# Optimization experiments

Measured on AMD Instinct MI355X. Metric: run time of the kernel, lower is better.

Reference implementation:

```python
import jax, jax.numpy as jnp
import numpy as np

D_MODEL = 1024
N_HEADS = 16
TREE_DEPTH = 5
B, T = 2, 1024


def setup_inputs() -> dict:
    key = jax.random.key(0)
    k1, k2, k3, k4 = jax.random.split(key, 4)
    sc = 1.0 / np.sqrt(D_MODEL)
    return {
        "x": jax.random.normal(k1, (B, T, D_MODEL), dtype=jnp.float32),
        "Wp": jax.random.normal(k2, (D_MODEL, N_HEADS * TREE_DEPTH), dtype=jnp.float32) * sc,
        "bp": jnp.zeros((N_HEADS * TREE_DEPTH,), dtype=jnp.float32),
        "Wv": jax.random.normal(k3, (D_MODEL, D_MODEL), dtype=jnp.float32) * sc,
        "Wo": jax.random.normal(k4, (D_MODEL, D_MODEL), dtype=jnp.float32) * sc,
    }


def reference(x, Wp, bp, Wv, Wo):
    Bc, Tc, d = x.shape
    H, Dt = N_HEADS, TREE_DEPTH
    dh = d // H
    # tree paths: (B, H, T, Dt)
    paths = jax.nn.sigmoid(x @ Wp + bp).reshape(Bc, Tc, H, Dt).transpose(0, 2, 1, 3)
    pq = paths[:, :, :, None, :]  # (B,H,T,1,Dt)
    pk = paths[:, :, None, :, :]  # (B,H,1,T,Dt)
    agree = pq * pk + (1.0 - pq) * (1.0 - pk)  # (B,H,T,T,Dt)
    sim = jnp.cumprod(agree, axis=-1).sum(axis=-1) / Dt  # (B,H,T,T)
    # causal mask (strict upper triangle -> -inf)
    causal_mask = jnp.triu(jnp.ones((Tc, Tc), dtype=bool), k=1)
    sim = jnp.where(causal_mask[None, None], -jnp.inf, sim)
    attn = jax.nn.softmax(sim, axis=-1)
    V = (x @ Wv).reshape(Bc, Tc, H, dh).transpose(0, 2, 1, 3)  # (B,H,T,dh)
    ctx = jnp.einsum("bhqk,bhkd->bhqd", attn, V)
    ctx = ctx.transpose(0, 2, 1, 3).reshape(Bc, Tc, d)
    return ctx @ Wo
```

## Files before the change

kernel.cpp:

```cpp
#include <hip/hip_runtime.h>
#include <hip/hip_bf16.h>

#define B_SZ 2
#define T_SEQ 1024
#define D_MODEL 1024
#define N_HEADS 16
#define TREE_DEPTH 5
#define DH 64

typedef __attribute__((ext_vector_type(8))) short short8;
typedef __attribute__((ext_vector_type(4))) float f32x4;

__device__ __forceinline__ ushort f2bf(float f) {
    uint32_t u = __float_as_uint(f);
    u += 0x7FFFu + ((u >> 16) & 1u);
    return (ushort)(u >> 16);
}

__device__ __forceinline__ void gll16(const void* g, void* l) {
    __builtin_amdgcn_global_load_lds(
        (const __attribute__((address_space(1))) void*)g,
        (__attribute__((address_space(3))) void*)l, 16, 0, 0);
}

__global__ __launch_bounds__(256) void prologue(
    const float* __restrict__ x, const float* __restrict__ Wv,
    const float* __restrict__ Wo, const float* __restrict__ Wp,
    ushort* __restrict__ xb, ushort* __restrict__ Wvt,
    ushort* __restrict__ Wot, ushort* __restrict__ Wpt)
{
    __shared__ __align__(16) char sm[20480];
    const int bid = blockIdx.x, tid = threadIdx.x;
    if (bid < 1024) {
        const int i = (bid * 256 + tid) * 8;
        const float4 a = *(const float4*)(x + i);
        const float4 b = *(const float4*)(x + i + 4);
        ushort o[8] = {f2bf(a.x), f2bf(a.y), f2bf(a.z), f2bf(a.w),
                       f2bf(b.x), f2bf(b.y), f2bf(b.z), f2bf(b.w)};
        *(uint4*)(xb + i) = *(const uint4*)o;
    } else if (bid < 3072) {
        const int t = bid - 1024;
        const float* W = (t < 1024) ? Wv : Wo;
        ushort* Wt = (t < 1024) ? Wvt : Wot;
        const int ti = t & 1023;
        const int n0 = (ti & 31) * 32, k0 = (ti >> 5) * 32;
        float (*tile)[33] = (float(*)[33])sm;
        const int tx = tid & 31, ty = tid >> 5;
        #pragma unroll
        for (int i = 0; i < 4; ++i)
            tile[ty + i * 8][tx] = W[(size_t)(k0 + ty + i * 8) * 1024 + n0 + tx];
        __syncthreads();
        #pragma unroll
        for (int i = 0; i < 4; ++i)
            Wt[(size_t)(n0 + ty + i * 8) * 1024 + k0 + tx] = f2bf(tile[tx][ty + i * 8]);
    } else {
        float* tile = (float*)sm;
        const int k0 = (bid - 3072) * 64;
        #pragma unroll
        for (int j = 0; j < 20; ++j) {
            const int i = tid + j * 256;
            tile[i] = Wp[(size_t)k0 * 80 + i];
        }
        __syncthreads();
        #pragma unroll
        for (int j = 0; j < 20; ++j) {
            const int o = tid + j * 256;
            const int n = o >> 6, k = o & 63;
            Wpt[(size_t)n * 1024 + k0 + k] = f2bf(tile[k * 80 + n]);
        }
    }
}

template <bool OUT_BF16>
__device__ __forceinline__ void gemm_body(
    const ushort* __restrict__ A, const ushort* __restrict__ Bt,
    void* __restrict__ Cv, int N, int K, int bx, int by,
    ushort* As, ushort* Bs)
{
    const int tid = threadIdx.x;
    const int lane = tid & 63;
    const int w = tid >> 6;
    const int wm = w & 1, wn = w >> 1;
    const int rowBase = by * 64;
    const int colBase = bx * 64;

    const int srow = lane & 15;
    const int sk = (lane >> 4) * 8;

    const ushort* gA = A + (size_t)(rowBase + w * 16 + srow) * K + sk;
    const ushort* gB = Bt + (size_t)(colBase + w * 16 + srow) * K + sk;

    f32x4 acc[2][2];
    #pragma unroll
    for (int i = 0; i < 2; ++i) {
        acc[i][0] = (f32x4)0.0f;
        acc[i][1] = (f32x4)0.0f;
    }

    gll16(gA,      As + (w * 2 + 0) * 512);
    gll16(gA + 32, As + (w * 2 + 1) * 512);
    gll16(gB,      Bs + (w * 2 + 0) * 512);
    gll16(gB + 32, Bs + (w * 2 + 1) * 512);

    const int niter = K / 64;
    for (int it = 0; it < niter; ++it) {
        __syncthreads();
        const int cur = (it & 1) * 4096;
        if (it + 1 < niter) {
            const int nxt = ((it + 1) & 1) * 4096;
            const int ko = (it + 1) * 64;
            gll16(gA + ko,      As + nxt + (w * 2 + 0) * 512);
            gll16(gA + ko + 32, As + nxt + (w * 2 + 1) * 512);
            gll16(gB + ko,      Bs + nxt + (w * 2 + 0) * 512);
            gll16(gB + ko + 32, Bs + nxt + (w * 2 + 1) * 512);
        }
        #pragma unroll
        for (int ks = 0; ks < 2; ++ks) {
            short8 af[2], bf[2];
            #pragma unroll
            for (int i = 0; i < 2; ++i)
                af[i] = *(const short8*)(As + cur + ((wm * 2 + i) * 2 + ks) * 512 + lane * 8);
            #pragma unroll
            for (int j = 0; j < 2; ++j)
                bf[j] = *(const short8*)(Bs + cur + ((wn * 2 + j) * 2 + ks) * 512 + lane * 8);
            #pragma unroll
            for (int i = 0; i < 2; ++i)
                #pragma unroll
                for (int j = 0; j < 2; ++j)
                    acc[i][j] = __builtin_amdgcn_mfma_f32_16x16x32_bf16(
                        af[i], bf[j], acc[i][j], 0, 0, 0);
        }
    }

    const int quad = lane >> 4, m16 = lane & 15;
    #pragma unroll
    for (int i = 0; i < 2; ++i)
        #pragma unroll
        for (int j = 0; j < 2; ++j) {
            const int col = colBase + wn * 32 + j * 16 + m16;
            #pragma unroll
            for (int r = 0; r < 4; ++r) {
                const int row = rowBase + wm * 32 + i * 16 + quad * 4 + r;
                if (OUT_BF16)
                    ((ushort*)Cv)[(size_t)row * N + col] = f2bf(acc[i][j][r]);
                else
                    ((float*)Cv)[(size_t)row * N + col] = acc[i][j][r];
            }
        }
}

__device__ __forceinline__ void phi_body(
    const ushort* __restrict__ xb, const ushort* __restrict__ Wpt,
    const float* __restrict__ bp, ushort* __restrict__ Phi,
    int blk, float* red, float* p_s)
{
    const int tid = threadIdx.x;
    const int lane = tid & 63, w = tid >> 6;
    const int quad = lane >> 4, m16 = lane & 15;
    const int row0 = blk * 16;

    f32x4 acc[5];
    #pragma unroll
    for (int nb = 0; nb < 5; ++nb) acc[nb] = (f32x4)0.0f;

    const ushort* ap = xb + (size_t)(row0 + m16) * 1024 + w * 256 + quad * 8;
    const ushort* bpz = Wpt + (size_t)m16 * 1024 + w * 256 + quad * 8;
    #pragma unroll
    for (int it = 0; it < 8; ++it) {
        const short8 af = *(const short8*)(ap + it * 32);
        #pragma unroll
        for (int nb = 0; nb < 5; ++nb) {
            const short8 bf = *(const short8*)(bpz + (size_t)nb * 16 * 1024 + it * 32);
            acc[nb] = __builtin_amdgcn_mfma_f32_16x16x32_bf16(af, bf, acc[nb], 0, 0, 0);
        }
    }
    #pragma unroll
    for (int nb = 0; nb < 5; ++nb)
        #pragma unroll
        for (int r = 0; r < 4; ++r)
            red[(w * 16 + quad * 4 + r) * 80 + nb * 16 + m16] = acc[nb][r];
    __syncthreads();
    #pragma unroll
    for (int j = 0; j < 5; ++j) {
        const int i = tid + j * 256;
        const int rr = i / 80, cc = i - rr * 80;
        const float v = red[(0 * 16 + rr) * 80 + cc] + red[(1 * 16 + rr) * 80 + cc] +
                        red[(2 * 16 + rr) * 80 + cc] + red[(3 * 16 + rr) * 80 + cc] + bp[cc];
        p_s[rr * 80 + cc] = 1.0f / (1.0f + __expf(-v));
    }
    __syncthreads();
    #pragma unroll
    for (int j = 0; j < 8; ++j) {
        const int c = tid + j * 256;
        const int rr = c >> 7, rem = c & 127;
        const int h = rem >> 3, f8 = (rem & 7) * 8;
        const float* pr = &p_s[rr * 80 + h * 5];
        ushort o[8];
        #pragma unroll
        for (int e = 0; e < 8; ++e) {
            const int f = f8 + e;
            float val = 0.0f;
            if (f < 62) {
                int d, off;
                if (f < 2)       { d = 1; off = 0; }
                else if (f < 6)  { d = 2; off = 2; }
                else if (f < 14) { d = 3; off = 6; }
                else if (f < 30) { d = 4; off = 14; }
                else             { d = 5; off = 30; }
                const int e2 = f - off;
                float prod = 1.0f;
                for (int jj = 1; jj <= d; ++jj) {
                    const float p = pr[jj - 1];
                    prod *= ((e2 >> (d - jj)) & 1) ? (1.0f - p) : p;
                }
                val = prod;
            }
            o[e] = f2bf(val);
        }
        const int grow = row0 + rr;
        const int b = grow >> 10, t = grow & 1023;
        *(uint4*)(Phi + ((size_t)(b * 16 + h) * 1024 + t) * 64 + f8) =
            *(const uint4*)o;
    }
}

__global__ __launch_bounds__(256) void mid_kernel(
    const ushort* __restrict__ xb, const ushort* __restrict__ Wvt,
    const ushort* __restrict__ Wpt, const float* __restrict__ bp,
    ushort* __restrict__ Vt, ushort* __restrict__ Phi)
{
    __shared__ __align__(16) char sm[32768];
    if (blockIdx.x < 512) {
        ushort* As = (ushort*)sm;
        ushort* Bs = As + 8192;
        gemm_body<true>(Wvt, xb, Vt, 2048, 1024,
                        blockIdx.x & 31, blockIdx.x >> 5, As, Bs);
    } else {
        float* red = (float*)sm;
        float* p_s = (float*)(sm + 20480);
        phi_body(xb, Wpt, bp, Phi, blockIdx.x - 512, red, p_s);
    }
}

__global__ __launch_bounds__(256) void gemm_out(
    const ushort* __restrict__ ctxb, const ushort* __restrict__ Wot,
    float* __restrict__ out)
{
    __shared__ __align__(16) ushort sm[16384];
    gemm_body<false>(ctxb, Wot, out, 1024, 1024,
                     blockIdx.x, blockIdx.y, sm, sm + 8192);
}

__global__ __launch_bounds__(256) void attn_mfma(
    const ushort* __restrict__ Phi, const ushort* __restrict__ Vt,
    ushort* __restrict__ ctxb)
{
    const int qt = 15 - blockIdx.x;
    const int bh = blockIdx.y;
    const int b = bh >> 4, h = bh & 15;
    const int tid = threadIdx.x;
    const int lane = tid & 63;
    const int w = tid >> 6;
    const int quad = lane >> 4, m16 = lane & 15;

    __shared__ __align__(16) ushort K_s[2][4096];
    __shared__ __align__(16) ushort V_s[2][4096];
    __shared__ __align__(16) ushort W_s[4096];
    __shared__ float den_s[4][16];

    const int srow = lane & 15;
    const int sk = (lane >> 4) * 8;
    const ushort* gK = Phi + (size_t)bh * 1024 * 64 + (w * 16 + srow) * 64 + sk;
    const ushort* gV = Vt + (size_t)(h * 64 + w * 16 + srow) * 2048 + b * 1024 + sk;

    const int qglob = qt * 64 + w * 16 + m16;
    const ushort* qbase = Phi + ((size_t)bh * 1024 + qglob) * 64 + quad * 8;
    const short8 qf0 = *(const short8*)qbase;
    const short8 qf1 = *(const short8*)(qbase + 32);

    f32x4 cacc[4];
    #pragma unroll
    for (int nb = 0; nb < 4; ++nb) cacc[nb] = (f32x4)0.0f;
    float den = 0.0f;

    gll16(gK,      K_s[0] + (w * 2 + 0) * 512);
    gll16(gK + 32, K_s[0] + (w * 2 + 1) * 512);
    gll16(gV,      V_s[0] + (w * 2 + 0) * 512);
    gll16(gV + 32, V_s[0] + (w * 2 + 1) * 512);

    for (int kt = 0; kt <= qt; ++kt) {
        const int cur = kt & 1;
        __syncthreads();
        if (kt < qt) {
            const int nxt = cur ^ 1;
            const ushort* nK = gK + (kt + 1) * 4096;
            const ushort* nV = gV + (kt + 1) * 64;
            gll16(nK,      K_s[nxt] + (w * 2 + 0) * 512);
            gll16(nK + 32, K_s[nxt] + (w * 2 + 1) * 512);
            gll16(nV,      V_s[nxt] + (w * 2 + 0) * 512);
            gll16(nV + 32, V_s[nxt] + (w * 2 + 1) * 512);
        }
        #pragma unroll
        for (int nb = 0; nb < 4; ++nb) {
            const short8 kf0 = *(const short8*)(K_s[cur] + (nb * 2 + 0) * 512 + lane * 8);
            const short8 kf1 = *(const short8*)(K_s[cur] + (nb * 2 + 1) * 512 + lane * 8);
            f32x4 s = (f32x4)0.0f;
            s = __builtin_amdgcn_mfma_f32_16x16x32_bf16(kf0, qf0, s, 0, 0, 0);
            s = __builtin_amdgcn_mfma_f32_16x16x32_bf16(kf1, qf1, s, 0, 0, 0);
            const int k0g = kt * 64 + nb * 16 + quad * 4;
            ushort o[4];
            #pragma unroll
            for (int r = 0; r < 4; ++r) {
                float wgt = 0.0f;
                if (k0g + r <= qglob) wgt = __expf(s[r] * 0.2f);
                den += wgt;
                o[r] = f2bf(wgt);
            }
            const int addr = (w * 2 + (nb >> 1)) * 512 +
                             ((nb & 1) * 2 + (quad >> 1)) * 128 +
                             m16 * 8 + (quad & 1) * 4;
            *(uint2*)(W_s + addr) = *(const uint2*)o;
        }
        __syncthreads();
        const short8 wf0 = *(const short8*)(W_s + (w * 2 + 0) * 512 + lane * 8);
        const short8 wf1 = *(const short8*)(W_s + (w * 2 + 1) * 512 + lane * 8);
        #pragma unroll
        for (int nb = 0; nb < 4; ++nb) {
            const short8 vf0 = *(const short8*)(V_s[cur] + (nb * 2 + 0) * 512 + lane * 8);
            const short8 vf1 = *(const short8*)(V_s[cur] + (nb * 2 + 1) * 512 + lane * 8);
            cacc[nb] = __builtin_amdgcn_mfma_f32_16x16x32_bf16(wf0, vf0, cacc[nb], 0, 0, 0);
            cacc[nb] = __builtin_amdgcn_mfma_f32_16x16x32_bf16(wf1, vf1, cacc[nb], 0, 0, 0);
        }
    }

    den += __shfl_xor(den, 16);
    den += __shfl_xor(den, 32);
    den_s[w][m16] = den;
    __syncthreads();
    float inv[4];
    #pragma unroll
    for (int r = 0; r < 4; ++r) inv[r] = 1.0f / den_s[w][quad * 4 + r];

    #pragma unroll
    for (int nb = 0; nb < 4; ++nb) {
        const int dim = h * 64 + nb * 16 + m16;
        #pragma unroll
        for (int r = 0; r < 4; ++r) {
            const int token = qt * 64 + w * 16 + quad * 4 + r;
            ctxb[(size_t)(b * 1024 + token) * D_MODEL + dim] = f2bf(cacc[nb][r] * inv[r]);
        }
    }
}

extern "C" void kernel_launch(void* const* d_in, const int* in_sizes, int n_in,
                              void* d_out, int out_size, void* d_ws, size_t ws_size,
                              hipStream_t stream)
{
    const float* x  = (const float*)d_in[0];
    const float* Wp = (const float*)d_in[1];
    const float* bp = (const float*)d_in[2];
    const float* Wv = (const float*)d_in[3];
    const float* Wo = (const float*)d_in[4];
    float* out = (float*)d_out;

    char* ws = (char*)d_ws;
    ushort* xb   = (ushort*)(ws);
    ushort* Wvt  = (ushort*)(ws + (4u  << 20));
    ushort* Wot  = (ushort*)(ws + (6u  << 20));
    ushort* Phi  = (ushort*)(ws + (8u  << 20));
    ushort* Vt   = (ushort*)(ws + (12u << 20));
    ushort* ctxb = (ushort*)(ws + (16u << 20));
    ushort* Wpt  = (ushort*)(ws + (20u << 20));

    prologue<<<3088, 256, 0, stream>>>(x, Wv, Wo, Wp, xb, Wvt, Wot, Wpt);
    mid_kernel<<<640, 256, 0, stream>>>(xb, Wvt, Wpt, bp, Vt, Phi);
    attn_mfma<<<dim3(16, 32), 256, 0, stream>>>(Phi, Vt, ctxb);
    gemm_out<<<dim3(16, 32), 256, 0, stream>>>(ctxb, Wot, out);
}
```

Baseline: 151.5 us.

## Fuse all four stages into one cooperative persistent kernel with grid syncs

Replaces the four separate launches (convert/transpose prologue, V-projection plus phi, attention, output GEMM) with one cooperative kernel of 512 blocks that loops over the work and separates stages with grid.sync(). The goal is to remove per-launch overhead and tail gaps between kernels. It also changes the attention tile order so each block gets a mix of long and short causal tiles. The cost is grid-wide barriers, a fixed grid of 512 that must stay co-resident (launch bounds request 2 blocks per CU), and uneven work in the mid stage, where blocks 384 and above run both a GEMM tile and the phi computation.

```diff
diff --git a/kernel.cpp b/kernel.cpp
--- a/kernel.cpp
+++ b/kernel.cpp
@@ -1,5 +1,6 @@
 #include <hip/hip_runtime.h>
 #include <hip/hip_bf16.h>
+#include <hip/hip_cooperative_groups.h>
 
 #define B_SZ 2
 #define T_SEQ 1024
@@ -21,54 +22,6 @@
     __builtin_amdgcn_global_load_lds(
         (const __attribute__((address_space(1))) void*)g,
         (__attribute__((address_space(3))) void*)l, 16, 0, 0);
-}
-
-__global__ __launch_bounds__(256) void prologue(
-    const float* __restrict__ x, const float* __restrict__ Wv,
-    const float* __restrict__ Wo, const float* __restrict__ Wp,
-    ushort* __restrict__ xb, ushort* __restrict__ Wvt,
-    ushort* __restrict__ Wot, ushort* __restrict__ Wpt)
-{
-    __shared__ __align__(16) char sm[20480];
-    const int bid = blockIdx.x, tid = threadIdx.x;
-    if (bid < 1024) {
-        const int i = (bid * 256 + tid) * 8;
-        const float4 a = *(const float4*)(x + i);
-        const float4 b = *(const float4*)(x + i + 4);
-        ushort o[8] = {f2bf(a.x), f2bf(a.y), f2bf(a.z), f2bf(a.w),
-                       f2bf(b.x), f2bf(b.y), f2bf(b.z), f2bf(b.w)};
-        *(uint4*)(xb + i) = *(const uint4*)o;
-    } else if (bid < 3072) {
-        const int t = bid - 1024;
-        const float* W = (t < 1024) ? Wv : Wo;
-        ushort* Wt = (t < 1024) ? Wvt : Wot;
-        const int ti = t & 1023;
-        const int n0 = (ti & 31) * 32, k0 = (ti >> 5) * 32;
-        float (*tile)[33] = (float(*)[33])sm;
-        const int tx = tid & 31, ty = tid >> 5;
-        #pragma unroll
-        for (int i = 0; i < 4; ++i)
-            tile[ty + i * 8][tx] = W[(size_t)(k0 + ty + i * 8) * 1024 + n0 + tx];
-        __syncthreads();
-        #pragma unroll
-        for (int i = 0; i < 4; ++i)
-            Wt[(size_t)(n0 + ty + i * 8) * 1024 + k0 + tx] = f2bf(tile[tx][ty + i * 8]);
-    } else {
-        float* tile = (float*)sm;
-        const int k0 = (bid - 3072) * 64;
-        #pragma unroll
-        for (int j = 0; j < 20; ++j) {
-            const int i = tid + j * 256;
-            tile[i] = Wp[(size_t)k0 * 80 + i];
-        }
-        __syncthreads();
-        #pragma unroll
-        for (int j = 0; j < 20; ++j) {
-            const int o = tid + j * 256;
-            const int n = o >> 6, k = o & 63;
-            Wpt[(size_t)n * 1024 + k0 + k] = f2bf(tile[k * 80 + n]);
-        }
-    }
 }
 
 template <bool OUT_BF16>
@@ -224,50 +177,17 @@
     }
 }
 
-__global__ __launch_bounds__(256) void mid_kernel(
-    const ushort* __restrict__ xb, const ushort* __restrict__ Wvt,
-    const ushort* __restrict__ Wpt, const float* __restrict__ bp,
-    ushort* __restrict__ Vt, ushort* __restrict__ Phi)
-{
-    __shared__ __align__(16) char sm[32768];
-    if (blockIdx.x < 512) {
-        ushort* As = (ushort*)sm;
-        ushort* Bs = As + 8192;
-        gemm_body<true>(Wvt, xb, Vt, 2048, 1024,
-                        blockIdx.x & 31, blockIdx.x >> 5, As, Bs);
-    } else {
-        float* red = (float*)sm;
-        float* p_s = (float*)(sm + 20480);
-        phi_body(xb, Wpt, bp, Phi, blockIdx.x - 512, red, p_s);
-    }
-}
-
-__global__ __launch_bounds__(256) void gemm_out(
-    const ushort* __restrict__ ctxb, const ushort* __restrict__ Wot,
-    float* __restrict__ out)
-{
-    __shared__ __align__(16) ushort sm[16384];
-    gemm_body<false>(ctxb, Wot, out, 1024, 1024,
-                     blockIdx.x, blockIdx.y, sm, sm + 8192);
-}
-
-__global__ __launch_bounds__(256) void attn_mfma(
+__device__ __forceinline__ void attn_body(
     const ushort* __restrict__ Phi, const ushort* __restrict__ Vt,
-    ushort* __restrict__ ctxb)
-{
-    const int qt = 15 - blockIdx.x;
-    const int bh = blockIdx.y;
+    ushort* __restrict__ ctxb, int qt, int bh,
+    ushort* K_s0, ushort* V_s0, ushort* W_s, float* den_s)
+{
     const int b = bh >> 4, h = bh & 15;
     const int tid = threadIdx.x;
     const int lane = tid & 63;
     const int w = tid >> 6;
     const int quad = lane >> 4, m16 = lane & 15;
 
-    __shared__ __align__(16) ushort K_s[2][4096];
-    __shared__ __align__(16) ushort V_s[2][4096];
-    __shared__ __align__(16) ushort W_s[4096];
-    __shared__ float den_s[4][16];
-
     const int srow = lane & 15;
     const int sk = (lane >> 4) * 8;
     const ushort* gK = Phi + (size_t)bh * 1024 * 64 + (w * 16 + srow) * 64 + sk;
@@ -283,27 +203,27 @@
     for (int nb = 0; nb < 4; ++nb) cacc[nb] = (f32x4)0.0f;
     float den = 0.0f;
 
-    gll16(gK,      K_s[0] + (w * 2 + 0) * 512);
-    gll16(gK + 32, K_s[0] + (w * 2 + 1) * 512);
-    gll16(gV,      V_s[0] + (w * 2 + 0) * 512);
-    gll16(gV + 32, V_s[0] + (w * 2 + 1) * 512);
+    gll16(gK,      K_s0 + (w * 2 + 0) * 512);
+    gll16(gK + 32, K_s0 + (w * 2 + 1) * 512);
+    gll16(gV,      V_s0 + (w * 2 + 0) * 512);
+    gll16(gV + 32, V_s0 + (w * 2 + 1) * 512);
 
     for (int kt = 0; kt <= qt; ++kt) {
-        const int cur = kt & 1;
+        const int cur = (kt & 1) * 4096;
         __syncthreads();
         if (kt < qt) {
-            const int nxt = cur ^ 1;
+            const int nxt = ((kt + 1) & 1) * 4096;
             const ushort* nK = gK + (kt + 1) * 4096;
             const ushort* nV = gV + (kt + 1) * 64;
-            gll16(nK,      K_s[nxt] + (w * 2 + 0) * 512);
-            gll16(nK + 32, K_s[nxt] + (w * 2 + 1) * 512);
-            gll16(nV,      V_s[nxt] + (w * 2 + 0) * 512);
-            gll16(nV + 32, V_s[nxt] + (w * 2 + 1) * 512);
+            gll16(nK,      K_s0 + nxt + (w * 2 + 0) * 512);
+            gll16(nK + 32, K_s0 + nxt + (w * 2 + 1) * 512);
+            gll16(nV,      V_s0 + nxt + (w * 2 + 0) * 512);
+            gll16(nV + 32, V_s0 + nxt + (w * 2 + 1) * 512);
         }
         #pragma unroll
         for (int nb = 0; nb < 4; ++nb) {
-            const short8 kf0 = *(const short8*)(K_s[cur] + (nb * 2 + 0) * 512 + lane * 8);
-            const short8 kf1 = *(const short8*)(K_s[cur] + (nb * 2 + 1) * 512 + lane * 8);
+            const short8 kf0 = *(const short8*)(K_s0 + cur + (nb * 2 + 0) * 512 + lane * 8);
+            const short8 kf1 = *(const short8*)(K_s0 + cur + (nb * 2 + 1) * 512 + lane * 8);
             f32x4 s = (f32x4)0.0f;
             s = __builtin_amdgcn_mfma_f32_16x16x32_bf16(kf0, qf0, s, 0, 0, 0);
             s = __builtin_amdgcn_mfma_f32_16x16x32_bf16(kf1, qf1, s, 0, 0, 0);
@@ -326,8 +246,8 @@
         const short8 wf1 = *(const short8*)(W_s + (w * 2 + 1) * 512 + lane * 8);
         #pragma unroll
         for (int nb = 0; nb < 4; ++nb) {
-            const short8 vf0 = *(const short8*)(V_s[cur] + (nb * 2 + 0) * 512 + lane * 8);
-            const short8 vf1 = *(const short8*)(V_s[cur] + (nb * 2 + 1) * 512 + lane * 8);
+            const short8 vf0 = *(const short8*)(V_s0 + cur + (nb * 2 + 0) * 512 + lane * 8);
+            const short8 vf1 = *(const short8*)(V_s0 + cur + (nb * 2 + 1) * 512 + lane * 8);
             cacc[nb] = __builtin_amdgcn_mfma_f32_16x16x32_bf16(wf0, vf0, cacc[nb], 0, 0, 0);
             cacc[nb] = __builtin_amdgcn_mfma_f32_16x16x32_bf16(wf1, vf1, cacc[nb], 0, 0, 0);
         }
@@ -335,11 +255,11 @@
 
     den += __shfl_xor(den, 16);
     den += __shfl_xor(den, 32);
-    den_s[w][m16] = den;
+    den_s[w * 16 + m16] = den;
     __syncthreads();
     float inv[4];
     #pragma unroll
-    for (int r = 0; r < 4; ++r) inv[r] = 1.0f / den_s[w][quad * 4 + r];
+    for (int r = 0; r < 4; ++r) inv[r] = 1.0f / den_s[w * 16 + quad * 4 + r];
 
     #pragma unroll
     for (int nb = 0; nb < 4; ++nb) {
@@ -349,6 +269,100 @@
             const int token = qt * 64 + w * 16 + quad * 4 + r;
             ctxb[(size_t)(b * 1024 + token) * D_MODEL + dim] = f2bf(cacc[nb][r] * inv[r]);
         }
+    }
+}
+
+__global__ __launch_bounds__(256, 2) void fused(
+    const float* __restrict__ x, const float* __restrict__ Wp,
+    const float* __restrict__ bp, const float* __restrict__ Wv,
+    const float* __restrict__ Wo,
+    ushort* __restrict__ xb, ushort* __restrict__ Wvt,
+    ushort* __restrict__ Wot, ushort* __restrict__ Wpt,
+    ushort* __restrict__ Phi, ushort* __restrict__ Vt,
+    ushort* __restrict__ ctxb, float* __restrict__ out)
+{
+    __shared__ __align__(16) char sm[41216];
+    cooperative_groups::grid_group grid = cooperative_groups::this_grid();
+    const int tid = threadIdx.x;
+
+    for (int u = blockIdx.x; u < 3088; u += 512) {
+        if (u < 1024) {
+            const int i = (u * 256 + tid) * 8;
+            const float4 a = *(const float4*)(x + i);
+            const float4 b = *(const float4*)(x + i + 4);
+            ushort o[8] = {f2bf(a.x), f2bf(a.y), f2bf(a.z), f2bf(a.w),
+                           f2bf(b.x), f2bf(b.y), f2bf(b.z), f2bf(b.w)};
+            *(uint4*)(xb + i) = *(const uint4*)o;
+        } else if (u < 3072) {
+            __syncthreads();
+            const int t = u - 1024;
+            const float* W = (t < 1024) ? Wv : Wo;
+            ushort* Wt = (t < 1024) ? Wvt : Wot;
+            const int ti = t & 1023;
+            const int n0 = (ti & 31) * 32, k0 = (ti >> 5) * 32;
+            float (*tile)[33] = (float(*)[33])sm;
+            const int tx = tid & 31, ty = tid >> 5;
+            #pragma unroll
+            for (int i = 0; i < 4; ++i)
+                tile[ty + i * 8][tx] = W[(size_t)(k0 + ty + i * 8) * 1024 + n0 + tx];
+            __syncthreads();
+            #pragma unroll
+            for (int i = 0; i < 4; ++i)
+                Wt[(size_t)(n0 + ty + i * 8) * 1024 + k0 + tx] =
+                    f2bf(tile[tx][ty + i * 8]);
+        } else {
+            __syncthreads();
+            float* tile = (float*)sm;
+            const int k0 = (u - 3072) * 64;
+            #pragma unroll
+            for (int j = 0; j < 20; ++j) {
+                const int i = tid + j * 256;
+                tile[i] = Wp[(size_t)k0 * 80 + i];
+            }
+            __syncthreads();
+            #pragma unroll
+            for (int j = 0; j < 20; ++j) {
+                const int o = tid + j * 256;
+                const int n = o >> 6, k = o & 63;
+                Wpt[(size_t)n * 1024 + k0 + k] = f2bf(tile[k * 80 + n]);
+            }
+        }
+    }
+    grid.sync();
+
+    {
+        ushort* As = (ushort*)sm;
+        ushort* Bs = As + 8192;
+        gemm_body<true>(Wvt, xb, Vt, 2048, 1024,
+                        blockIdx.x & 31, blockIdx.x >> 5, As, Bs);
+        if (blockIdx.x >= 384) {
+            __syncthreads();
+            float* red = (float*)sm;
+            float* p_s = (float*)(sm + 20480);
+            phi_body(xb, Wpt, bp, Phi, blockIdx.x - 384, red, p_s);
+        }
+    }
+    grid.sync();
+
+    {
+        const int i = blockIdx.x;
+        const int s = (i >> 1) & 15;
+        const int flip = (i ^ (i >> 8)) & 1;
+        const int qt = flip ? 15 - s : s;
+        const int bh = ((i >> 5) & 15) | ((i & 1) << 4);
+        ushort* K_s = (ushort*)sm;
+        ushort* V_s = (ushort*)(sm + 16384);
+        ushort* W_s = (ushort*)(sm + 32768);
+        float* den_s = (float*)(sm + 40960);
+        attn_body(Phi, Vt, ctxb, qt, bh, K_s, V_s, W_s, den_s);
+    }
+    grid.sync();
+
+    {
+        ushort* As = (ushort*)sm;
+        ushort* Bs = As + 8192;
+        gemm_body<false>(ctxb, Wot, out, 1024, 1024,
+                         blockIdx.x & 15, blockIdx.x >> 4, As, Bs);
     }
 }
 
@@ -372,8 +386,8 @@
     ushort* ctxb = (ushort*)(ws + (16u << 20));
     ushort* Wpt  = (ushort*)(ws + (20u << 20));
 
-    prologue<<<3088, 256, 0, stream>>>(x, Wv, Wo, Wp, xb, Wvt, Wot, Wpt);
-    mid_kernel<<<640, 256, 0, stream>>>(xb, Wvt, Wpt, bp, Vt, Phi);
-    attn_mfma<<<dim3(16, 32), 256, 0, stream>>>(Phi, Vt, ctxb);
-    gemm_out<<<dim3(16, 32), 256, 0, stream>>>(ctxb, Wot, out);
-}
+    void* args[] = {&x, &Wp, &bp, &Wv, &Wo,
+                    &xb, &Wvt, &Wot, &Wpt, &Phi, &Vt, &ctxb, &out};
+    hipLaunchCooperativeKernel((void*)fused, dim3(512), dim3(256),
+                               args, 0, stream);
+}
```

After: 337.9 us. 2.23x slower.
